# Kernel tuning notes

Hardware: AMD Instinct MI355X
Metric: run time of the kernel (lower is better)

The kernel has to match this reference:

```python
import jax, jax.numpy as jnp
import numpy as np


def _tsallis15_probs(x):
    """entmax-1.5 / Tsallis alpha=1.5 mapping over axis=1. x: [n, d] logits."""
    x = (x - jnp.max(x, axis=1, keepdims=True)) * 0.5
    xs = -jnp.sort(-x, axis=1)                       # descending sort  [n, d]
    d = x.shape[1]
    rho = jnp.arange(1, d + 1, dtype=x.dtype)        # 1..d
    mean = jnp.cumsum(xs, axis=1) / rho
    mean_sq = jnp.cumsum(xs * xs, axis=1) / rho
    ss = rho * (mean_sq - mean * mean)
    delta = (1.0 - ss) / rho
    tau = mean - jnp.sqrt(jnp.clip(delta, 0.0))
    support_size = jnp.sum(tau <= xs, axis=1)        # [n]
    tau_star = jnp.take_along_axis(tau, (support_size - 1)[:, None], axis=1)
    y = jnp.clip(x - tau_star, 0.0)
    return y * y                                     # p*, rows sum to 1


def setup_inputs() -> dict:
    key = jax.random.key(0)
    k1, k2 = jax.random.split(key)
    inp = jax.random.normal(k1, (2048, 32000), dtype=jnp.float32)
    target = jax.random.randint(k2, (2048,), 0, 32000, dtype=jnp.int64)
    return {"input": inp, "target": target}


def reference(input, target):
    n = input.shape[0]
    p_star = _tsallis15_probs(input)
    # omega_tsallis15: (1 - sum p^{3/2}) / 0.75 per row
    loss = (1.0 - jnp.sum(p_star * jnp.sqrt(p_star), axis=1)) / 0.75
    # scatter_add(-1) at the target class, then <p* - e_y, x> per row
    pm = p_star.at[jnp.arange(n), target].add(-1.0)
    loss = loss + jnp.einsum('ij,ij->i', pm, input)
    # reduction='elementwise_mean', ignore_index=-100 (<0: no masking)
    return jnp.sum(loss) / n
```

## Files before the change

### kernel.cpp

```cpp
#include <hip/hip_runtime.h>
#include <math.h>

#define BLOCK 1024
#define NWAVES (BLOCK / 64)
#define NV 8
#define CAND_CAP 6144
#define NREG 12

__device__ __forceinline__ float waveReduceMax(float v) {
#pragma unroll
    for (int off = 32; off > 0; off >>= 1)
        v = fmaxf(v, __shfl_down(v, off, 64));
    return v;
}
__device__ __forceinline__ float waveReduceSum(float v) {
#pragma unroll
    for (int off = 32; off > 0; off >>= 1)
        v += __shfl_down(v, off, 64);
    return v;
}

__global__ __launch_bounds__(BLOCK, 8) void tsallis15_kernel(
    const float* __restrict__ x, const int* __restrict__ tgt,
    float* __restrict__ out, int n, int d, float inv_n)
{
    __shared__ float s_cand[CAND_CAP];
    __shared__ float s_red[NWAVES];
    __shared__ int   s_cnt;
    __shared__ float s_bcast;

    const int row  = blockIdx.x;
    const int t    = threadIdx.x;
    const int lane = t & 63;
    const int wave = t >> 6;
    const float* __restrict__ xr = x + (size_t)row * (size_t)d;

    if (t == 0) s_cnt = 0;

    float xt = 0.0f;
    if (t == 0) xt = xr[tgt[row]];

    float4 r[NV];
#pragma unroll
    for (int i = 0; i < NV; ++i) {
        int e = (i * BLOCK + t) * 4;
        if (e + 4 <= d) {
            r[i] = *reinterpret_cast<const float4*>(xr + e);
        } else {
            float4 v = make_float4(-INFINITY, -INFINITY, -INFINITY, -INFINITY);
            if (e < d)     v.x = xr[e];
            if (e + 1 < d) v.y = xr[e + 1];
            if (e + 2 < d) v.z = xr[e + 2];
            r[i] = v;
        }
    }

    float m = -INFINITY;
#pragma unroll
    for (int i = 0; i < NV; ++i)
        m = fmaxf(m, fmaxf(fmaxf(r[i].x, r[i].y), fmaxf(r[i].z, r[i].w)));
    m = waveReduceMax(m);
    if (lane == 0) s_red[wave] = m;
    __syncthreads();
    if (wave == 0) {
        float v = (lane < NWAVES) ? s_red[lane] : -INFINITY;
        v = waveReduceMax(v);
        if (lane == 0) s_bcast = v;
    }
    __syncthreads();
    const float rowmax = s_bcast;

    const float thr = rowmax - 2.0f;
#pragma unroll
    for (int i = 0; i < NV; ++i) {
        float vals[4] = { r[i].x, r[i].y, r[i].z, r[i].w };
#pragma unroll
        for (int c = 0; c < 4; ++c) {
            float v = vals[c];
            bool pred = (v >= thr);
            unsigned long long mask = __ballot(pred);
            if (mask) {
                int base;
                if (lane == 0) base = atomicAdd(&s_cnt, __popcll(mask));
                base = __shfl(base, 0, 64);
                if (pred) {
                    int pos = base + (int)__popcll(mask & ((1ull << lane) - 1ull));
                    if (pos < CAND_CAP) s_cand[pos] = (v - rowmax) * 0.5f;
                }
            }
        }
    }
    __syncthreads();

    if (wave == 0) {
        const int k = min(s_cnt, CAND_CAP);

        float ur[NREG];
#pragma unroll
        for (int j = 0; j < NREG; ++j) {
            int idx = lane + 64 * j;
            ur[j] = (idx < k) ? s_cand[idx] : -1e30f;
        }

        float lo = -1.0f, hi = 0.0f;
        for (int it = 0; it < 18; ++it) {
            float tau = 0.5f * (lo + hi);
            float acc = 0.0f;
#pragma unroll
            for (int j = 0; j < NREG; ++j) {
                float u = ur[j] - tau;
                acc += (u > 0.0f) ? u * u : 0.0f;
            }
            for (int j = 64 * NREG + lane; j < k; j += 64) {
                float u = s_cand[j] - tau;
                if (u > 0.0f) acc += u * u;
            }
            float tot = waveReduceSum(acc);
            tot = __shfl(tot, 0, 64);
            if (tot >= 1.0f) lo = tau; else hi = tau;
        }
        const float tau_b = 0.5f * (lo + hi);

        float s1 = 0.0f, s2 = 0.0f, sc = 0.0f;
#pragma unroll
        for (int j = 0; j < NREG; ++j) {
            float u = ur[j];
            if (u > tau_b) { s1 += u; s2 += u * u; sc += 1.0f; }
        }
        for (int j = 64 * NREG + lane; j < k; j += 64) {
            float u = s_cand[j];
            if (u > tau_b) { s1 += u; s2 += u * u; sc += 1.0f; }
        }
        s1 = waveReduceSum(s1); s1 = __shfl(s1, 0, 64);
        s2 = waveReduceSum(s2); s2 = __shfl(s2, 0, 64);
        sc = waveReduceSum(sc); sc = __shfl(sc, 0, 64);
        float mean  = s1 / sc;
        float ss    = s2 - s1 * mean;
        float delta = (1.0f - ss) / sc;
        if (delta < 0.0f) delta = 0.0f;
        const float tau_star = mean - sqrtf(delta);

        float p32 = 0.0f, dot = 0.0f;
#pragma unroll
        for (int j = 0; j < NREG; ++j) {
            float u = ur[j] - tau_star;
            if (u > 0.0f) {
                float p = u * u;
                p32 += p * u;
                dot += p * (2.0f * ur[j] + rowmax);
            }
        }
        for (int j = 64 * NREG + lane; j < k; j += 64) {
            float uc = s_cand[j];
            float u  = uc - tau_star;
            if (u > 0.0f) {
                float p = u * u;
                p32 += p * u;
                dot += p * (2.0f * uc + rowmax);
            }
        }
        p32 = waveReduceSum(p32);
        dot = waveReduceSum(dot);
        if (lane == 0) {
            float loss = (1.0f - p32) * (4.0f / 3.0f) + dot - xt;
            atomicAdd(out, loss * inv_n);
        }
    }
}

extern "C" void kernel_launch(void* const* d_in, const int* in_sizes, int n_in,
                              void* d_out, int out_size, void* d_ws, size_t ws_size,
                              hipStream_t stream) {
    const float* x   = (const float*)d_in[0];
    const int*   tgt = (const int*)d_in[1];
    float*       out = (float*)d_out;

    const int n = in_sizes[1];
    const int d = in_sizes[0] / n;

    hipMemsetAsync(out, 0, (size_t)out_size * sizeof(float), stream);
    tsallis15_kernel<<<n, BLOCK, 0, stream>>>(x, tgt, out, n, d, 1.0f / (float)n);
}
```

Baseline: 372.3 us.

## Split row processing into chunked candidate-filter pass and per-row solve pass

Replaces the single one-block-per-row kernel with two kernels. The first splits each row into 8K-element chunks, filters candidates against a chunk-local max minus 2, and appends them to a per-row workspace buffer. The second recomputes the row max from the candidates and runs the bisection solve, falling back to a full row rescan when a buffer overflows. The goal is more parallelism and better bandwidth from many small blocks instead of 2048 large ones, at the cost of an extra launch, workspace traffic, and more candidates kept because the thresholds are chunk-local.

```diff
diff --git a/kernel.cpp b/kernel.cpp
--- a/kernel.cpp
+++ b/kernel.cpp
@@ -1,24 +1,315 @@
 #include <hip/hip_runtime.h>
 #include <math.h>
+
+__device__ __forceinline__ float waveReduceMax(float v) {
+#pragma unroll
+    for (int off = 32; off > 0; off >>= 1)
+        v = fmaxf(v, __shfl_down(v, off, 64));
+    return v;
+}
+__device__ __forceinline__ float waveReduceSum(float v) {
+#pragma unroll
+    for (int off = 32; off > 0; off >>= 1)
+        v += __shfl_down(v, off, 64);
+    return v;
+}
+
+#define NREG 12
+__device__ __forceinline__ void solve_wave0(const float* s_cand, int k,
+                                            float rowmax, float xt,
+                                            float inv_n, float* out, int lane)
+{
+    float ur[NREG];
+#pragma unroll
+    for (int j = 0; j < NREG; ++j) {
+        int idx = lane + 64 * j;
+        ur[j] = (idx < k) ? s_cand[idx] : -1e30f;
+    }
+
+    float lo = -1.0f, hi = 0.0f;
+    for (int it = 0; it < 18; ++it) {
+        float tau = 0.5f * (lo + hi);
+        float acc = 0.0f;
+#pragma unroll
+        for (int j = 0; j < NREG; ++j) {
+            float u = ur[j] - tau;
+            acc += (u > 0.0f) ? u * u : 0.0f;
+        }
+        for (int j = 64 * NREG + lane; j < k; j += 64) {
+            float u = s_cand[j] - tau;
+            if (u > 0.0f) acc += u * u;
+        }
+        float tot = waveReduceSum(acc);
+        tot = __shfl(tot, 0, 64);
+        if (tot >= 1.0f) lo = tau; else hi = tau;
+    }
+    const float tau_b = 0.5f * (lo + hi);
+
+    float s1 = 0.0f, s2 = 0.0f, sc = 0.0f;
+#pragma unroll
+    for (int j = 0; j < NREG; ++j) {
+        float u = ur[j];
+        if (u > tau_b) { s1 += u; s2 += u * u; sc += 1.0f; }
+    }
+    for (int j = 64 * NREG + lane; j < k; j += 64) {
+        float u = s_cand[j];
+        if (u > tau_b) { s1 += u; s2 += u * u; sc += 1.0f; }
+    }
+    s1 = waveReduceSum(s1); s1 = __shfl(s1, 0, 64);
+    s2 = waveReduceSum(s2); s2 = __shfl(s2, 0, 64);
+    sc = waveReduceSum(sc); sc = __shfl(sc, 0, 64);
+    float mean  = s1 / sc;
+    float ss    = s2 - s1 * mean;
+    float delta = (1.0f - ss) / sc;
+    if (delta < 0.0f) delta = 0.0f;
+    const float tau_star = mean - sqrtf(delta);
+
+    float p32 = 0.0f, dot = 0.0f;
+#pragma unroll
+    for (int j = 0; j < NREG; ++j) {
+        float u = ur[j] - tau_star;
+        if (u > 0.0f) {
+            float p = u * u;
+            p32 += p * u;
+            dot += p * (2.0f * ur[j] + rowmax);
+        }
+    }
+    for (int j = 64 * NREG + lane; j < k; j += 64) {
+        float uc = s_cand[j];
+        float u  = uc - tau_star;
+        if (u > 0.0f) {
+            float p = u * u;
+            p32 += p * u;
+            dot += p * (2.0f * uc + rowmax);
+        }
+    }
+    p32 = waveReduceSum(p32);
+    dot = waveReduceSum(dot);
+    if (lane == 0) {
+        float loss = (1.0f - p32) * (4.0f / 3.0f) + dot - xt;
+        atomicAdd(out, loss * inv_n);
+    }
+}
+
+#define P1_BLOCK 256
+#define P1_NV 8
+#define CHUNK4 (P1_BLOCK * P1_NV)
+#define P1_LDSCAP 2048
+#define CAP_WS 4096
+
+__global__ __launch_bounds__(P1_BLOCK, 8) void tsallis15_pass1(
+    const float* __restrict__ x, float* __restrict__ cand,
+    int* __restrict__ cnt, int* __restrict__ ovf, int n, int d, int cpr)
+{
+    __shared__ float s_c[P1_LDSCAP];
+    __shared__ float s_red[4];
+    __shared__ float s_bcast;
+    __shared__ int   s_k, s_base;
+
+    const int bid  = blockIdx.x;
+    const int row  = bid / cpr;
+    const int chk  = bid - row * cpr;
+    const int t    = threadIdx.x;
+    const int lane = t & 63;
+    const int wave = t >> 6;
+    const int d4   = d >> 2;
+    const float* __restrict__ xr = x + (size_t)row * (size_t)d;
+    const float4* __restrict__ xr4 = reinterpret_cast<const float4*>(xr);
+    const int c0 = chk * CHUNK4;
+    const bool last = (chk == cpr - 1);
+
+    if (t == 0) s_k = 0;
+
+    float4 r[P1_NV];
+#pragma unroll
+    for (int j = 0; j < P1_NV; ++j) {
+        int idx = c0 + t + j * P1_BLOCK;
+        r[j] = (idx < d4) ? xr4[idx]
+                          : make_float4(-INFINITY, -INFINITY, -INFINITY, -INFINITY);
+    }
+    float tailv = -INFINITY;
+    if (last) {
+        int e = (d4 << 2) + t;
+        if (e < d) tailv = xr[e];
+    }
+
+    float m = tailv;
+#pragma unroll
+    for (int j = 0; j < P1_NV; ++j)
+        m = fmaxf(m, fmaxf(fmaxf(r[j].x, r[j].y), fmaxf(r[j].z, r[j].w)));
+    m = waveReduceMax(m);
+    if (lane == 0) s_red[wave] = m;
+    __syncthreads();
+    if (wave == 0) {
+        float v = (lane < 4) ? s_red[lane] : -INFINITY;
+        v = waveReduceMax(v);
+        if (lane == 0) s_bcast = v;
+    }
+    __syncthreads();
+    const float thr = s_bcast - 2.0f;
+
+#pragma unroll
+    for (int j = 0; j < P1_NV; ++j) {
+        float4 v = r[j];
+        float mx4 = fmaxf(fmaxf(v.x, v.y), fmaxf(v.z, v.w));
+        unsigned long long any = __ballot(mx4 >= thr);
+        if (any) {
+            float vals[4] = { v.x, v.y, v.z, v.w };
+#pragma unroll
+            for (int c = 0; c < 4; ++c) {
+                float vv = vals[c];
+                bool pred = (vv >= thr);
+                unsigned long long mask = __ballot(pred);
+                if (mask) {
+                    int base;
+                    if (lane == 0) base = atomicAdd(&s_k, __popcll(mask));
+                    base = __shfl(base, 0, 64);
+                    if (pred) {
+                        int pos = base + (int)__popcll(mask & ((1ull << lane) - 1ull));
+                        if (pos < P1_LDSCAP) s_c[pos] = vv;
+                    }
+                }
+            }
+        }
+    }
+    {
+        bool pred = (tailv >= thr);
+        unsigned long long mask = __ballot(pred);
+        if (mask) {
+            int base;
+            if (lane == 0) base = atomicAdd(&s_k, __popcll(mask));
+            base = __shfl(base, 0, 64);
+            if (pred) {
+                int pos = base + (int)__popcll(mask & ((1ull << lane) - 1ull));
+                if (pos < P1_LDSCAP) s_c[pos] = tailv;
+            }
+        }
+    }
+    __syncthreads();
+
+    const int k = min(s_k, P1_LDSCAP);
+    if (t == 0) {
+        s_base = atomicAdd(&cnt[row], k);
+        if (s_k > P1_LDSCAP) atomicOr(&ovf[row], 1);
+    }
+    __syncthreads();
+    const int base = s_base;
+    for (int i = t; i < k; i += P1_BLOCK) {
+        int pos = base + i;
+        if (pos < CAP_WS) cand[(size_t)row * CAP_WS + pos] = s_c[i];
+    }
+    if (t == 0 && base + k > CAP_WS) atomicOr(&ovf[row], 1);
+}
+
+#define P2_CAP 6144
+__global__ __launch_bounds__(P1_BLOCK, 4) void tsallis15_pass2(
+    const float* __restrict__ x, const int* __restrict__ tgt,
+    const float* __restrict__ cand, const int* __restrict__ cnt,
+    const int* __restrict__ ovf, float* __restrict__ out,
+    int n, int d, float inv_n)
+{
+    __shared__ float s_cand[P2_CAP];
+    __shared__ float s_red[4];
+    __shared__ float s_bcast;
+    __shared__ int   s_k;
+
+    const int row  = blockIdx.x;
+    const int t    = threadIdx.x;
+    const int lane = t & 63;
+    const int wave = t >> 6;
+    const int d4   = d >> 2;
+    const float* __restrict__ xr = x + (size_t)row * (size_t)d;
+
+    float xt = 0.0f;
+    if (t == 0) xt = xr[tgt[row]];
+
+    int k;
+    if (ovf[row] == 0) {
+        k = min(cnt[row], CAP_WS);
+        const float* rl = cand + (size_t)row * CAP_WS;
+        float m = -INFINITY;
+        for (int i = t; i < k; i += P1_BLOCK) {
+            float v = rl[i];
+            s_cand[i] = v;
+            m = fmaxf(m, v);
+        }
+        m = waveReduceMax(m);
+        if (lane == 0) s_red[wave] = m;
+        __syncthreads();
+        if (wave == 0) {
+            float v = (lane < 4) ? s_red[lane] : -INFINITY;
+            v = waveReduceMax(v);
+            if (lane == 0) s_bcast = v;
+        }
+        __syncthreads();
+        const float rowmax = s_bcast;
+        for (int i = t; i < k; i += P1_BLOCK)
+            s_cand[i] = (s_cand[i] - rowmax) * 0.5f;
+        __syncthreads();
+        if (wave == 0) solve_wave0(s_cand, k, rowmax, xt, inv_n, out, lane);
+    } else {
+        const float4* xr4 = reinterpret_cast<const float4*>(xr);
+        float m = -INFINITY;
+        for (int i = t; i < d4; i += P1_BLOCK) {
+            float4 v = xr4[i];
+            m = fmaxf(m, fmaxf(fmaxf(v.x, v.y), fmaxf(v.z, v.w)));
+        }
+        { int e = (d4 << 2) + t; if (e < d) m = fmaxf(m, xr[e]); }
+        m = waveReduceMax(m);
+        if (lane == 0) s_red[wave] = m;
+        __syncthreads();
+        if (wave == 0) {
+            float v = (lane < 4) ? s_red[lane] : -INFINITY;
+            v = waveReduceMax(v);
+            if (lane == 0) s_bcast = v;
+        }
+        if (t == 0) s_k = 0;
+        __syncthreads();
+        const float rowmax = s_bcast;
+        const float thr = rowmax - 2.0f;
+        for (int i = t; i < d4; i += P1_BLOCK) {
+            float4 v = xr4[i];
+            float vals[4] = { v.x, v.y, v.z, v.w };
+#pragma unroll
+            for (int c = 0; c < 4; ++c) {
+                float vv = vals[c];
+                bool pred = (vv >= thr);
+                unsigned long long mask = __ballot(pred);
+                if (mask) {
+                    int base;
+                    if (lane == 0) base = atomicAdd(&s_k, __popcll(mask));
+                    base = __shfl(base, 0, 64);
+                    if (pred) {
+                        int pos = base + (int)__popcll(mask & ((1ull << lane) - 1ull));
+                        if (pos < P2_CAP) s_cand[pos] = (vv - rowmax) * 0.5f;
+                    }
+                }
+            }
+        }
+        {   int e = (d4 << 2) + t;
+            float vv = (e < d) ? xr[e] : -INFINITY;
+            bool pred = (vv >= thr);
+            unsigned long long mask = __ballot(pred);
+            if (mask) {
+                int base;
+                if (lane == 0) base = atomicAdd(&s_k, __popcll(mask));
+                base = __shfl(base, 0, 64);
+                if (pred) {
+                    int pos = base + (int)__popcll(mask & ((1ull << lane) - 1ull));
+                    if (pos < P2_CAP) s_cand[pos] = (vv - rowmax) * 0.5f;
+                }
+            }
+        }
+        __syncthreads();
+        k = min(s_k, P2_CAP);
+        if (wave == 0) solve_wave0(s_cand, k, rowmax, xt, inv_n, out, lane);
+    }
+}
 
 #define BLOCK 1024
 #define NWAVES (BLOCK / 64)
 #define NV 8
 #define CAND_CAP 6144
-#define NREG 12
-
-__device__ __forceinline__ float waveReduceMax(float v) {
-#pragma unroll
-    for (int off = 32; off > 0; off >>= 1)
-        v = fmaxf(v, __shfl_down(v, off, 64));
-    return v;
-}
-__device__ __forceinline__ float waveReduceSum(float v) {
-#pragma unroll
-    for (int off = 32; off > 0; off >>= 1)
-        v += __shfl_down(v, off, 64);
-    return v;
-}
 
 __global__ __launch_bounds__(BLOCK, 8) void tsallis15_kernel(
     const float* __restrict__ x, const int* __restrict__ tgt,
@@ -36,7 +327,6 @@
     const float* __restrict__ xr = x + (size_t)row * (size_t)d;
 
     if (t == 0) s_cnt = 0;
-
     float xt = 0.0f;
     if (t == 0) xt = xr[tgt[row]];
 
@@ -94,77 +384,7 @@
 
     if (wave == 0) {
         const int k = min(s_cnt, CAND_CAP);
-
-        float ur[NREG];
-#pragma unroll
-        for (int j = 0; j < NREG; ++j) {
-            int idx = lane + 64 * j;
-            ur[j] = (idx < k) ? s_cand[idx] : -1e30f;
-        }
-
-        float lo = -1.0f, hi = 0.0f;
-        for (int it = 0; it < 18; ++it) {
-            float tau = 0.5f * (lo + hi);
-            float acc = 0.0f;
-#pragma unroll
-            for (int j = 0; j < NREG; ++j) {
-                float u = ur[j] - tau;
-                acc += (u > 0.0f) ? u * u : 0.0f;
-            }
-            for (int j = 64 * NREG + lane; j < k; j += 64) {
-                float u = s_cand[j] - tau;
-                if (u > 0.0f) acc += u * u;
-            }
-            float tot = waveReduceSum(acc);
-            tot = __shfl(tot, 0, 64);
-            if (tot >= 1.0f) lo = tau; else hi = tau;
-        }
-        const float tau_b = 0.5f * (lo + hi);
-
-        float s1 = 0.0f, s2 = 0.0f, sc = 0.0f;
-#pragma unroll
-        for (int j = 0; j < NREG; ++j) {
-            float u = ur[j];
-            if (u > tau_b) { s1 += u; s2 += u * u; sc += 1.0f; }
-        }
-        for (int j = 64 * NREG + lane; j < k; j += 64) {
-            float u = s_cand[j];
-            if (u > tau_b) { s1 += u; s2 += u * u; sc += 1.0f; }
-        }
-        s1 = waveReduceSum(s1); s1 = __shfl(s1, 0, 64);
-        s2 = waveReduceSum(s2); s2 = __shfl(s2, 0, 64);
-        sc = waveReduceSum(sc); sc = __shfl(sc, 0, 64);
-        float mean  = s1 / sc;
-        float ss    = s2 - s1 * mean;
-        float delta = (1.0f - ss) / sc;
-        if (delta < 0.0f) delta = 0.0f;
-        const float tau_star = mean - sqrtf(delta);
-
-        float p32 = 0.0f, dot = 0.0f;
-#pragma unroll
-        for (int j = 0; j < NREG; ++j) {
-            float u = ur[j] - tau_star;
-            if (u > 0.0f) {
-                float p = u * u;
-                p32 += p * u;
-                dot += p * (2.0f * ur[j] + rowmax);
-            }
-        }
-        for (int j = 64 * NREG + lane; j < k; j += 64) {
-            float uc = s_cand[j];
-            float u  = uc - tau_star;
-            if (u > 0.0f) {
-                float p = u * u;
-                p32 += p * u;
-                dot += p * (2.0f * uc + rowmax);
-            }
-        }
-        p32 = waveReduceSum(p32);
-        dot = waveReduceSum(dot);
-        if (lane == 0) {
-            float loss = (1.0f - p32) * (4.0f / 3.0f) + dot - xt;
-            atomicAdd(out, loss * inv_n);
-        }
+        solve_wave0(s_cand, k, rowmax, xt, inv_n, out, lane);
     }
 }
 
@@ -177,7 +397,24 @@
 
     const int n = in_sizes[1];
     const int d = in_sizes[0] / n;
+    const float inv_n = 1.0f / (float)n;
 
     hipMemsetAsync(out, 0, (size_t)out_size * sizeof(float), stream);
-    tsallis15_kernel<<<n, BLOCK, 0, stream>>>(x, tgt, out, n, d, 1.0f / (float)n);
-}
+
+    const int d4  = d >> 2;
+    int cpr = (d4 + CHUNK4 - 1) / CHUNK4;
+    if (cpr < 1) cpr = 1;
+    const size_t need = (size_t)n * 8 + (size_t)n * CAP_WS * 4;
+    const long long nblk = (long long)n * (long long)cpr;
+
+    if (d_ws && ws_size >= need && nblk <= 0x7FFFFFFFLL) {
+        int*   cnt  = (int*)d_ws;
+        int*   ovf  = cnt + n;
+        float* cand = (float*)(ovf + n);
+        hipMemsetAsync(d_ws, 0, (size_t)n * 8, stream);
+        tsallis15_pass1<<<(int)nblk, P1_BLOCK, 0, stream>>>(x, cand, cnt, ovf, n, d, cpr);
+        tsallis15_pass2<<<n, P1_BLOCK, 0, stream>>>(x, tgt, cand, cnt, ovf, out, n, d, inv_n);
+    } else {
+        tsallis15_kernel<<<n, BLOCK, 0, stream>>>(x, tgt, out, n, d, inv_n);
+    }
+}
```

Measured after the change: 417.3 us. +12.1%, slower.

## Make kernel persistent with double-buffered register prefetch of next row

Applied to the files above, without the earlier changes.

The grid shrinks to at most 256 blocks, and each block loops over rows with a stride of the grid size. While a block processes the current row, it issues the global loads for the next row into a second register buffer, so memory latency overlaps with the reduction, candidate collection and the serial wave-0 solve. Target logits for the first 64 rows a block handles are gathered up front by wave 0. The block's __syncthreads calls become raw s_waitcnt plus s_barrier, and the launch-bounds occupancy hint drops from 8 to 4; both buffers live in registers, which raises register pressure.

```diff
diff --git a/kernel.cpp b/kernel.cpp
--- a/kernel.cpp
+++ b/kernel.cpp
@@ -7,6 +7,8 @@
 #define CAND_CAP 6144
 #define NREG 12
 
+#define BAR() asm volatile("s_waitcnt lgkmcnt(0)\n\ts_barrier" ::: "memory")
+
 __device__ __forceinline__ float waveReduceMax(float v) {
 #pragma unroll
     for (int off = 32; off > 0; off >>= 1)
@@ -20,27 +22,8 @@
     return v;
 }
 
-__global__ __launch_bounds__(BLOCK, 8) void tsallis15_kernel(
-    const float* __restrict__ x, const int* __restrict__ tgt,
-    float* __restrict__ out, int n, int d, float inv_n)
-{
-    __shared__ float s_cand[CAND_CAP];
-    __shared__ float s_red[NWAVES];
-    __shared__ int   s_cnt;
-    __shared__ float s_bcast;
-
-    const int row  = blockIdx.x;
-    const int t    = threadIdx.x;
-    const int lane = t & 63;
-    const int wave = t >> 6;
-    const float* __restrict__ xr = x + (size_t)row * (size_t)d;
-
-    if (t == 0) s_cnt = 0;
-
-    float xt = 0.0f;
-    if (t == 0) xt = xr[tgt[row]];
-
-    float4 r[NV];
+__device__ __forceinline__ void issue_row_load(const float* __restrict__ xr,
+                                               int t, int d, float4 (&r)[NV]) {
 #pragma unroll
     for (int i = 0; i < NV; ++i) {
         int e = (i * BLOCK + t) * 4;
@@ -51,26 +34,110 @@
             if (e < d)     v.x = xr[e];
             if (e + 1 < d) v.y = xr[e + 1];
             if (e + 2 < d) v.z = xr[e + 2];
+            if (e + 3 < d) v.w = xr[e + 3];
             r[i] = v;
         }
     }
-
+}
+
+__device__ __forceinline__ void solve_wave0(const float* s_cand, int k,
+                                            float rowmax, float xt,
+                                            float inv_n, float* out, int lane)
+{
+    float ur[NREG];
+#pragma unroll
+    for (int j = 0; j < NREG; ++j) {
+        int idx = lane + 64 * j;
+        ur[j] = (idx < k) ? s_cand[idx] : -1e30f;
+    }
+
+    float lo = -1.0f, hi = 0.0f;
+    for (int it = 0; it < 18; ++it) {
+        float tau = 0.5f * (lo + hi);
+        float acc = 0.0f;
+#pragma unroll
+        for (int j = 0; j < NREG; ++j) {
+            float u = ur[j] - tau;
+            acc += (u > 0.0f) ? u * u : 0.0f;
+        }
+        for (int j = 64 * NREG + lane; j < k; j += 64) {
+            float u = s_cand[j] - tau;
+            if (u > 0.0f) acc += u * u;
+        }
+        float tot = waveReduceSum(acc);
+        tot = __shfl(tot, 0, 64);
+        if (tot >= 1.0f) lo = tau; else hi = tau;
+    }
+    const float tau_b = 0.5f * (lo + hi);
+
+    float s1 = 0.0f, s2 = 0.0f, sc = 0.0f;
+#pragma unroll
+    for (int j = 0; j < NREG; ++j) {
+        float u = ur[j];
+        if (u > tau_b) { s1 += u; s2 += u * u; sc += 1.0f; }
+    }
+    for (int j = 64 * NREG + lane; j < k; j += 64) {
+        float u = s_cand[j];
+        if (u > tau_b) { s1 += u; s2 += u * u; sc += 1.0f; }
+    }
+    s1 = waveReduceSum(s1); s1 = __shfl(s1, 0, 64);
+    s2 = waveReduceSum(s2); s2 = __shfl(s2, 0, 64);
+    sc = waveReduceSum(sc); sc = __shfl(sc, 0, 64);
+    float mean  = s1 / sc;
+    float ss    = s2 - s1 * mean;
+    float delta = (1.0f - ss) / sc;
+    if (delta < 0.0f) delta = 0.0f;
+    const float tau_star = mean - sqrtf(delta);
+
+    float p32 = 0.0f, dot = 0.0f;
+#pragma unroll
+    for (int j = 0; j < NREG; ++j) {
+        float u = ur[j] - tau_star;
+        if (u > 0.0f) {
+            float p = u * u;
+            p32 += p * u;
+            dot += p * (2.0f * ur[j] + rowmax);
+        }
+    }
+    for (int j = 64 * NREG + lane; j < k; j += 64) {
+        float uc = s_cand[j];
+        float u  = uc - tau_star;
+        if (u > 0.0f) {
+            float p = u * u;
+            p32 += p * u;
+            dot += p * (2.0f * uc + rowmax);
+        }
+    }
+    p32 = waveReduceSum(p32);
+    dot = waveReduceSum(dot);
+    if (lane == 0) {
+        float loss = (1.0f - p32) * (4.0f / 3.0f) + dot - xt;
+        atomicAdd(out, loss * inv_n);
+    }
+}
+
+__device__ __forceinline__ void process_row(
+    const float4 (&r)[NV], float xt, float inv_n,
+    int t, int lane, int wave,
+    float* s_cand, float* s_red, int* s_cnt, float* s_bcast,
+    float* __restrict__ out)
+{
     float m = -INFINITY;
 #pragma unroll
     for (int i = 0; i < NV; ++i)
         m = fmaxf(m, fmaxf(fmaxf(r[i].x, r[i].y), fmaxf(r[i].z, r[i].w)));
     m = waveReduceMax(m);
     if (lane == 0) s_red[wave] = m;
-    __syncthreads();
+    BAR();
     if (wave == 0) {
         float v = (lane < NWAVES) ? s_red[lane] : -INFINITY;
         v = waveReduceMax(v);
-        if (lane == 0) s_bcast = v;
-    }
-    __syncthreads();
-    const float rowmax = s_bcast;
-
+        if (lane == 0) *s_bcast = v;
+    }
+    BAR();
+    const float rowmax = *s_bcast;
     const float thr = rowmax - 2.0f;
+
 #pragma unroll
     for (int i = 0; i < NV; ++i) {
         float vals[4] = { r[i].x, r[i].y, r[i].z, r[i].w };
@@ -81,7 +148,7 @@
             unsigned long long mask = __ballot(pred);
             if (mask) {
                 int base;
-                if (lane == 0) base = atomicAdd(&s_cnt, __popcll(mask));
+                if (lane == 0) base = atomicAdd(s_cnt, __popcll(mask));
                 base = __shfl(base, 0, 64);
                 if (pred) {
                     int pos = base + (int)__popcll(mask & ((1ull << lane) - 1ull));
@@ -90,80 +157,61 @@
             }
         }
     }
-    __syncthreads();
+    BAR();
 
     if (wave == 0) {
-        const int k = min(s_cnt, CAND_CAP);
-
-        float ur[NREG];
-#pragma unroll
-        for (int j = 0; j < NREG; ++j) {
-            int idx = lane + 64 * j;
-            ur[j] = (idx < k) ? s_cand[idx] : -1e30f;
-        }
-
-        float lo = -1.0f, hi = 0.0f;
-        for (int it = 0; it < 18; ++it) {
-            float tau = 0.5f * (lo + hi);
-            float acc = 0.0f;
-#pragma unroll
-            for (int j = 0; j < NREG; ++j) {
-                float u = ur[j] - tau;
-                acc += (u > 0.0f) ? u * u : 0.0f;
-            }
-            for (int j = 64 * NREG + lane; j < k; j += 64) {
-                float u = s_cand[j] - tau;
-                if (u > 0.0f) acc += u * u;
-            }
-            float tot = waveReduceSum(acc);
-            tot = __shfl(tot, 0, 64);
-            if (tot >= 1.0f) lo = tau; else hi = tau;
-        }
-        const float tau_b = 0.5f * (lo + hi);
-
-        float s1 = 0.0f, s2 = 0.0f, sc = 0.0f;
-#pragma unroll
-        for (int j = 0; j < NREG; ++j) {
-            float u = ur[j];
-            if (u > tau_b) { s1 += u; s2 += u * u; sc += 1.0f; }
-        }
-        for (int j = 64 * NREG + lane; j < k; j += 64) {
-            float u = s_cand[j];
-            if (u > tau_b) { s1 += u; s2 += u * u; sc += 1.0f; }
-        }
-        s1 = waveReduceSum(s1); s1 = __shfl(s1, 0, 64);
-        s2 = waveReduceSum(s2); s2 = __shfl(s2, 0, 64);
-        sc = waveReduceSum(sc); sc = __shfl(sc, 0, 64);
-        float mean  = s1 / sc;
-        float ss    = s2 - s1 * mean;
-        float delta = (1.0f - ss) / sc;
-        if (delta < 0.0f) delta = 0.0f;
-        const float tau_star = mean - sqrtf(delta);
-
-        float p32 = 0.0f, dot = 0.0f;
-#pragma unroll
-        for (int j = 0; j < NREG; ++j) {
-            float u = ur[j] - tau_star;
-            if (u > 0.0f) {
-                float p = u * u;
-                p32 += p * u;
-                dot += p * (2.0f * ur[j] + rowmax);
-            }
-        }
-        for (int j = 64 * NREG + lane; j < k; j += 64) {
-            float uc = s_cand[j];
-            float u  = uc - tau_star;
-            if (u > 0.0f) {
-                float p = u * u;
-                p32 += p * u;
-                dot += p * (2.0f * uc + rowmax);
-            }
-        }
-        p32 = waveReduceSum(p32);
-        dot = waveReduceSum(dot);
-        if (lane == 0) {
-            float loss = (1.0f - p32) * (4.0f / 3.0f) + dot - xt;
-            atomicAdd(out, loss * inv_n);
+        const int k = min(*s_cnt, CAND_CAP);
+        if (lane == 0) *s_cnt = 0;
+        solve_wave0(s_cand, k, rowmax, xt, inv_n, out, lane);
+    }
+}
+
+__global__ __launch_bounds__(BLOCK, 4) void tsallis15_kernel(
+    const float* __restrict__ x, const int* __restrict__ tgt,
+    float* __restrict__ out, int n, int d, float inv_n)
+{
+    __shared__ float s_cand[CAND_CAP];
+    __shared__ float s_red[NWAVES];
+    __shared__ int   s_cnt;
+    __shared__ float s_bcast;
+
+    const int t    = threadIdx.x;
+    const int lane = t & 63;
+    const int wave = t >> 6;
+    const int grid = gridDim.x;
+    const int row0 = blockIdx.x;
+
+    if (t == 0) s_cnt = 0;
+
+    float4 bufA[NV], bufB[NV];
+    issue_row_load(x + (size_t)row0 * (size_t)d, t, d, bufA);
+
+    float xt_pre = 0.0f;
+    if (wave == 0) {
+        int rr = row0 + lane * grid;
+        if (rr < n) xt_pre = x[(size_t)rr * (size_t)d + tgt[rr]];
+    }
+
+    int iter = 0;
+    for (int row = row0; row < n; row += grid, ++iter) {
+        const int nextrow = row + grid;
+        float xt;
+        if (iter < 64) {
+            xt = __shfl(xt_pre, iter, 64);
+        } else {
+            xt = 0.0f;
+            if (t == 0) xt = x[(size_t)row * (size_t)d + tgt[row]];
+        }
+        if ((iter & 1) == 0) {
+            if (nextrow < n)
+                issue_row_load(x + (size_t)nextrow * (size_t)d, t, d, bufB);
+            process_row(bufA, xt, inv_n, t, lane, wave,
+                        s_cand, s_red, &s_cnt, &s_bcast, out);
+        } else {
+            if (nextrow < n)
+                issue_row_load(x + (size_t)nextrow * (size_t)d, t, d, bufA);
+            process_row(bufB, xt, inv_n, t, lane, wave,
+                        s_cand, s_red, &s_cnt, &s_bcast, out);
         }
     }
 }
@@ -179,5 +227,6 @@
     const int d = in_sizes[0] / n;
 
     hipMemsetAsync(out, 0, (size_t)out_size * sizeof(float), stream);
-    tsallis15_kernel<<<n, BLOCK, 0, stream>>>(x, tgt, out, n, d, 1.0f / (float)n);
-}
+    const int grid = (n < 256) ? n : 256;
+    tsallis15_kernel<<<grid, BLOCK, 0, stream>>>(x, tgt, out, n, d, 1.0f / (float)n);
+}
```

Result: slower. 501.4 us (+34.7%).
